# Performance work log

Hardware: AMD Instinct MI355X
Metric: run time of the kernel (lower is better)

The kernel has to match this reference:

```python
import jax, jax.numpy as jnp
import numpy as np

B, S, H, C = 2, 128, 768, 5
NEG = -1024.0

def setup_inputs() -> dict:
    key = jax.random.key(0)
    ks = jax.random.split(key, 6)
    sequence_output = jax.random.normal(ks[0], (B, S, H), dtype=jnp.float32)
    attention_mask = jnp.ones((B, S), dtype=jnp.int32)
    ng_token_mask = jax.random.bernoulli(ks[1], 0.5, (B, S, C, S))  # bool
    target = (jax.random.uniform(ks[2], (B, S, C, S)) < 0.01).astype(jnp.float32)
    lim = 1.0 / np.sqrt(H)
    W_prd = jax.random.uniform(ks[3], (H, H), jnp.float32, -lim, lim)
    b_prd = jnp.zeros((H,), jnp.float32)
    W_arg = jax.random.uniform(ks[4], (C * H, H), jnp.float32, -lim, lim)
    b_arg = jnp.zeros((C * H,), jnp.float32)
    W_out = jax.random.uniform(ks[5], (C, H), jnp.float32, -lim, lim)
    return dict(sequence_output=sequence_output, attention_mask=attention_mask,
                ng_token_mask=ng_token_mask, target=target,
                W_prd=W_prd, b_prd=b_prd, W_arg=W_arg, b_arg=b_arg, W_out=W_out)

def reference(sequence_output, attention_mask, ng_token_mask, target,
              W_prd, b_prd, W_arg, b_arg, W_out):
    b, s, h = sequence_output.shape
    c = W_out.shape[0]
    # get_mask: ng mask restricted to attended tokens, then any over case dim
    mask = ng_token_mask & (attention_mask[:, None, None, :] > 0)   # (B,S,C,S)
    mask = jnp.any(mask, axis=2, keepdims=True)                      # (B,S,1,S)
    # dropout is identity in eval mode
    h_p = sequence_output @ W_prd.T + b_prd                          # (B,S,H)
    h_a = (sequence_output @ W_arg.T + b_arg).reshape(b, s, c, h)    # (B,S,C,H)
    # outer-sum biaffine: (B, S_prd, S_arg, C, H)
    hh = jnp.tanh(h_p[:, :, None, None, :] + h_a[:, None, :, :, :])
    # per-case Linear(H,1,bias=False), stacked at dim=2 -> (B, S_prd, C, S_arg)
    output = jnp.einsum('bpach,ch->bpca', hh, W_out)
    output = output + (~mask).astype(output.dtype) * NEG
    # cross_entropy_pas_loss: multi-hot CE over candidate (last) axis
    log_sm = jax.nn.log_softmax(output, axis=3)
    loss = jnp.sum(-log_sm * target) / jnp.sum(target)
    return loss, output
```

## Files before the change

### kernel.cpp

```cpp
#include <hip/hip_runtime.h>
#include <math.h>

#define Bb 2
#define Ss 128
#define Hh 768
#define Cc 5
#define Mm 256
#define NEGV -1024.0f
#define SCALE 2.8853900817779268f

#define PT 2
#define NBLK (Mm / PT * Cc)

typedef __attribute__((ext_vector_type(8))) short bf16x8;
typedef __attribute__((ext_vector_type(4))) float f32x4;
typedef unsigned short ushort;

__device__ __forceinline__ unsigned pack_hi16(float hi, float lo) {
    return (__float_as_uint(hi) & 0xFFFF0000u) | (__float_as_uint(lo) >> 16);
}
__device__ __forceinline__ bf16x8 pack_bf16x8(float4 lo, float4 hi) {
    union { bf16x8 v; unsigned u[4]; } r;
    r.u[0] = pack_hi16(lo.y, lo.x);
    r.u[1] = pack_hi16(lo.w, lo.z);
    r.u[2] = pack_hi16(hi.y, hi.x);
    r.u[3] = pack_hi16(hi.w, hi.z);
    return r.v;
}

#define SB __builtin_amdgcn_sched_barrier(0);

__global__ __launch_bounds__(256)
void gemm_mfma(const float* __restrict__ X,
               const float* __restrict__ Wprd,
               const float* __restrict__ Warg,
               const float* __restrict__ bprd,
               const float* __restrict__ barg,
               float* __restrict__ EpG,
               ushort* __restrict__ haTb,
               float* __restrict__ accum)
{
    __shared__ __align__(16) ushort Asb[64][40];
    __shared__ __align__(16) ushort Bsb[32][40];

    if (blockIdx.x == 0 && blockIdx.y == 0 && threadIdx.x == 0) {
        accum[0] = 0.f; accum[1] = 0.f;
        ((unsigned*)accum)[2] = 0u;
    }
    const int bm   = blockIdx.x;
    const int bn   = blockIdx.y;
    const int tid  = threadIdx.x;
    const int wave = tid >> 6;
    const int lane = tid & 63;
    const int l16  = lane & 15;
    const int quad = lane >> 4;

    const float* Wsrc; const float* bsrc;
    const int nb = bn * 32;
    if (nb < Hh) { Wsrc = Wprd + (size_t)nb * Hh;        bsrc = bprd + nb; }
    else         { Wsrc = Warg + (size_t)(nb - Hh) * Hh; bsrc = barg + (nb - Hh); }

    const int srow = tid >> 2;
    const int sko  = (tid & 3) * 8;
    const float* gA = X + (size_t)(bm * 64 + srow) * Hh + sko;
    const float* gB = Wsrc + (size_t)(tid >> 2) * Hh + sko;

    float4 pa0 = *(const float4*)(gA);
    float4 pa1 = *(const float4*)(gA + 4);
    float4 pb0, pb1;
    if (tid < 128) { pb0 = *(const float4*)(gB); pb1 = *(const float4*)(gB + 4); }

    f32x4 acc0 = {0.f,0.f,0.f,0.f}, acc1 = {0.f,0.f,0.f,0.f};

    for (int k0 = 0; k0 < Hh; k0 += 32) {
        *(bf16x8*)&Asb[srow][sko] = pack_bf16x8(pa0, pa1);
        if (tid < 128) *(bf16x8*)&Bsb[tid >> 2][sko] = pack_bf16x8(pb0, pb1);
        __syncthreads();
        const int kn = k0 + 32;
        if (kn < Hh) {
            pa0 = *(const float4*)(gA + kn);
            pa1 = *(const float4*)(gA + kn + 4);
            if (tid < 128) { pb0 = *(const float4*)(gB + kn); pb1 = *(const float4*)(gB + kn + 4); }
        }
        bf16x8 af = *(const bf16x8*)&Asb[wave * 16 + l16][quad * 8];
        bf16x8 b0 = *(const bf16x8*)&Bsb[l16][quad * 8];
        bf16x8 b1 = *(const bf16x8*)&Bsb[16 + l16][quad * 8];
        acc0 = __builtin_amdgcn_mfma_f32_16x16x32_bf16(af, b0, acc0, 0, 0, 0);
        acc1 = __builtin_amdgcn_mfma_f32_16x16x32_bf16(af, b1, acc1, 0, 0, 0);
        __syncthreads();
    }

    const float sb0 = SCALE * bsrc[l16];
    const float sb1 = SCALE * bsrc[16 + l16];
    const int row = bm * 64 + wave * 16 + quad * 4;

    if (nb < Hh) {
        #pragma unroll
        for (int r = 0; r < 4; ++r) {
            const int mm = row + r;
            EpG[(size_t)mm * Hh + nb + l16]      = __builtin_amdgcn_exp2f(SCALE * acc0[r] + sb0);
            EpG[(size_t)mm * Hh + nb + 16 + l16] = __builtin_amdgcn_exp2f(SCALE * acc1[r] + sb1);
        }
    } else {
        const int q  = nb - Hh;
        const int cU = q / Hh;
        const int h0 = q % Hh;
        const int hA = h0 + l16;
        const int hB = h0 + 16 + l16;
        const size_t offA = (size_t)(hA >> 3) * 1024 + (hA & 7);
        const size_t offB = (size_t)(hB >> 3) * 1024 + (hB & 7);
        #pragma unroll
        for (int r = 0; r < 4; ++r) {
            const int mm = row + r;
            const int bI = mm >> 7, aI = mm & 127;
            const size_t base = ((size_t)(bI * Cc + cU) * 96) * 1024 + (size_t)aI * 8;
            const float v0 = SCALE * acc0[r] + sb0;
            const float v1 = SCALE * acc1[r] + sb1;
            haTb[base + offA] = (ushort)(__float_as_uint(v0) >> 16);
            haTb[base + offB] = (ushort)(__float_as_uint(v1) >> 16);
        }
    }
}

#define LOADG4(R, g) \
    R##0 = hap4[((g)*4+0)*128]; R##1 = hap4[((g)*4+1)*128]; \
    R##2 = hap4[((g)*4+2)*128]; R##3 = hap4[((g)*4+3)*128];

#define C1(u, hx) { \
    float w8[8], q0[8], q1[8]; \
    _Pragma("unroll") \
    for (int z = 0; z < 8; ++z) { \
        w8[z] = wrow[(hx) + z]; q0[z] = ep0[(hx) + z]; q1[z] = ep1[(hx) + z]; \
    } \
    const float e0 = __builtin_amdgcn_exp2f(__uint_as_float((u).x << 16)); \
    const float e1 = __builtin_amdgcn_exp2f(__uint_as_float((u).x & 0xFFFF0000u)); \
    const float e2 = __builtin_amdgcn_exp2f(__uint_as_float((u).y << 16)); \
    const float e3 = __builtin_amdgcn_exp2f(__uint_as_float((u).y & 0xFFFF0000u)); \
    const float e4 = __builtin_amdgcn_exp2f(__uint_as_float((u).z << 16)); \
    const float e5 = __builtin_amdgcn_exp2f(__uint_as_float((u).z & 0xFFFF0000u)); \
    const float e6 = __builtin_amdgcn_exp2f(__uint_as_float((u).w << 16)); \
    const float e7 = __builtin_amdgcn_exp2f(__uint_as_float((u).w & 0xFFFF0000u)); \
    float r; \
    r = __builtin_amdgcn_rcpf(fmaf(q0[0], e0, 1.0f)); ac00 = fmaf(w8[0], r, ac00); \
    r = __builtin_amdgcn_rcpf(fmaf(q0[1], e1, 1.0f)); ac01 = fmaf(w8[1], r, ac01); \
    r = __builtin_amdgcn_rcpf(fmaf(q0[2], e2, 1.0f)); ac00 = fmaf(w8[2], r, ac00); \
    r = __builtin_amdgcn_rcpf(fmaf(q0[3], e3, 1.0f)); ac01 = fmaf(w8[3], r, ac01); \
    r = __builtin_amdgcn_rcpf(fmaf(q0[4], e4, 1.0f)); ac00 = fmaf(w8[4], r, ac00); \
    r = __builtin_amdgcn_rcpf(fmaf(q0[5], e5, 1.0f)); ac01 = fmaf(w8[5], r, ac01); \
    r = __builtin_amdgcn_rcpf(fmaf(q0[6], e6, 1.0f)); ac00 = fmaf(w8[6], r, ac00); \
    r = __builtin_amdgcn_rcpf(fmaf(q0[7], e7, 1.0f)); ac01 = fmaf(w8[7], r, ac01); \
    r = __builtin_amdgcn_rcpf(fmaf(q1[0], e0, 1.0f)); ac10 = fmaf(w8[0], r, ac10); \
    r = __builtin_amdgcn_rcpf(fmaf(q1[1], e1, 1.0f)); ac11 = fmaf(w8[1], r, ac11); \
    r = __builtin_amdgcn_rcpf(fmaf(q1[2], e2, 1.0f)); ac10 = fmaf(w8[2], r, ac10); \
    r = __builtin_amdgcn_rcpf(fmaf(q1[3], e3, 1.0f)); ac11 = fmaf(w8[3], r, ac11); \
    r = __builtin_amdgcn_rcpf(fmaf(q1[4], e4, 1.0f)); ac10 = fmaf(w8[4], r, ac10); \
    r = __builtin_amdgcn_rcpf(fmaf(q1[5], e5, 1.0f)); ac11 = fmaf(w8[5], r, ac11); \
    r = __builtin_amdgcn_rcpf(fmaf(q1[6], e6, 1.0f)); ac10 = fmaf(w8[6], r, ac10); \
    r = __builtin_amdgcn_rcpf(fmaf(q1[7], e7, 1.0f)); ac11 = fmaf(w8[7], r, ac11); \
}

#define CONSUMEG4(R, g) \
    C1(R##0, hbase + ((g)*4+0)*8)  C1(R##1, hbase + ((g)*4+1)*8) \
    C1(R##2, hbase + ((g)*4+2)*8)  C1(R##3, hbase + ((g)*4+3)*8)

__global__ __launch_bounds__(512, 6)
void biaffine_loss(const float* __restrict__ EpG,
                   const ushort* __restrict__ haTb,
                   const float* __restrict__ Wout,
                   const int* __restrict__ ng,
                   const int* __restrict__ att,
                   const float* __restrict__ target,
                   float* __restrict__ out_logits,
                   float* __restrict__ accum,
                   float* __restrict__ out_loss)
{
    __shared__ float partial[PT][3][Ss];
    __shared__ float maskneg[PT][Ss];
    __shared__ float redmax[PT][2];
    __shared__ float red3[PT][2][3];
    __shared__ float swr_s;

    const int pt  = blockIdx.x / Cc;
    const int c   = blockIdx.x - pt * Cc;
    const int bp0 = pt * PT;
    const int b   = bp0 >> 7;
    const int tid = threadIdx.x;
    const int a   = tid & (Ss - 1);
    const int hq  = __builtin_amdgcn_readfirstlane(tid >> 7);
    const int lane = tid & 63;

    const float* wrow = Wout + (size_t)c * Hh;
    const float* ep0  = EpG + (size_t)(bp0 + 0) * Hh;
    const float* ep1  = EpG + (size_t)(bp0 + 1) * Hh;

    if (tid < PT * Ss) {
        const int p_i = tid >> 7;
        const int aa  = tid & (Ss - 1);
        int any = 0;
        if (att[b * Ss + aa] > 0) {
            const int* ngp = ng + (size_t)(bp0 + p_i) * Cc * Ss + aa;
            #pragma unroll
            for (int cc = 0; cc < Cc; ++cc) any |= ngp[cc * Ss];
        }
        maskneg[p_i][aa] = any ? 0.0f : NEGV;
    }

    if (tid < 64) {
        float s = 0.f;
        #pragma unroll
        for (int i = 0; i < Hh / 64; ++i) s += wrow[tid + i * 64];
        #pragma unroll
        for (int off = 32; off; off >>= 1) s += __shfl_xor(s, off, 64);
        if (tid == 0) swr_s = s;
    }

    const uint4* hap4 = (const uint4*)(haTb + ((size_t)(b * Cc + c) * 96) * 1024)
                      + (size_t)hq * 24 * 128 + a;
    const int hbase = hq * 192;

    uint4 A0, A1, A2, A3;
    uint4 B0, B1, B2, B3;
    float ac00 = 0.f, ac01 = 0.f, ac10 = 0.f, ac11 = 0.f;

    LOADG4(A, 0) SB
    LOADG4(B, 1) SB  CONSUMEG4(A, 0) SB
    LOADG4(A, 2) SB  CONSUMEG4(B, 1) SB
    LOADG4(B, 3) SB  CONSUMEG4(A, 2) SB
    LOADG4(A, 4) SB  CONSUMEG4(B, 3) SB
    LOADG4(B, 5) SB  CONSUMEG4(A, 4) SB
    CONSUMEG4(B, 5)

    if (hq != 0) {
        partial[0][hq - 1][a] = ac00 + ac01;
        partial[1][hq - 1][a] = ac10 + ac11;
    }
    __syncthreads();

    float logit[PT];
    const int wv = tid >> 6;
    if (hq == 0) {
        const float ps[PT] = { ac00 + ac01, ac10 + ac11 };
        #pragma unroll
        for (int p = 0; p < PT; ++p) {
            const float full = ps[p] + partial[p][0][a] + partial[p][1][a] + partial[p][2][a];
            logit[p] = swr_s - 2.0f * full + maskneg[p][a];
            out_logits[((size_t)(bp0 + p) * Cc + c) * Ss + a] = logit[p];
            float mx = logit[p];
            #pragma unroll
            for (int off = 32; off; off >>= 1) mx = fmaxf(mx, __shfl_xor(mx, off, 64));
            if (lane == 0) redmax[p][wv] = mx;
        }
    }
    __syncthreads();

    if (hq == 0) {
        #pragma unroll
        for (int p = 0; p < PT; ++p) {
            const float rm = fmaxf(redmax[p][0], redmax[p][1]);
            const float e  = __builtin_amdgcn_exp2f((logit[p] - rm) * 1.4426950408889634f);
            const float tg = target[((size_t)(bp0 + p) * Cc + c) * Ss + a];
            float se = e, st = tg, sx = tg * logit[p];
            #pragma unroll
            for (int off = 32; off; off >>= 1) {
                se += __shfl_xor(se, off, 64);
                st += __shfl_xor(st, off, 64);
                sx += __shfl_xor(sx, off, 64);
            }
            if (lane == 0) { red3[p][wv][0] = se; red3[p][wv][1] = st; red3[p][wv][2] = sx; }
        }
    }
    __syncthreads();

    if (tid == 0) {
        float nsum = 0.f, dsum = 0.f;
        #pragma unroll
        for (int p = 0; p < PT; ++p) {
            const float rm = fmaxf(redmax[p][0], redmax[p][1]);
            const float SE = red3[p][0][0] + red3[p][1][0];
            const float ST = red3[p][0][1] + red3[p][1][1];
            const float SX = red3[p][0][2] + red3[p][1][2];
            const float lse = rm + __builtin_amdgcn_logf(SE) * 0.6931471805599453f;
            nsum += lse * ST - SX;
            dsum += ST;
        }
        atomicAdd(&accum[0], nsum);
        atomicAdd(&accum[1], dsum);
        __threadfence();
        const unsigned old = atomicAdd((unsigned*)(accum + 2), 1u);
        if (old == (unsigned)(NBLK - 1)) {
            const float n = atomicAdd(&accum[0], 0.0f);
            const float d = atomicAdd(&accum[1], 0.0f);
            out_loss[0] = n / d;
        }
    }
}

extern "C" void kernel_launch(void* const* d_in, const int* in_sizes, int n_in,
                              void* d_out, int out_size, void* d_ws, size_t ws_size,
                              hipStream_t stream) {
    const float* seq    = (const float*)d_in[0];
    const int*   att    = (const int*)  d_in[1];
    const int*   ng     = (const int*)  d_in[2];
    const float* target = (const float*)d_in[3];
    const float* Wprd   = (const float*)d_in[4];
    const float* bprd   = (const float*)d_in[5];
    const float* Warg   = (const float*)d_in[6];
    const float* barg   = (const float*)d_in[7];
    const float* Wout   = (const float*)d_in[8];

    float*  out    = (float*)d_out;
    float*  EpG    = (float*)d_ws;
    ushort* haTb   = (ushort*)(EpG + 196608);
    float*  accum  = EpG + 196608 + 491520;

    gemm_mfma<<<dim3(4, 144), 256, 0, stream>>>(seq, Wprd, Warg, bprd, barg,
                                                EpG, haTb, accum);
    biaffine_loss<<<dim3(NBLK), 512, 0, stream>>>(EpG, haTb, Wout, ng, att, target,
                                                  out + 1, accum, out);
}
```

Before: 134.5 us.

## Precompute exp of arg projection in GEMM epilogue and double-buffer GEMM k-loop

The GEMM epilogue now stores exp2(scaled h_a) rounded to bf16 (round-to-nearest-even), so the biaffine inner loop no longer evaluates exp2 per element and only unpacks the bf16 values. This moves the exponential from the S×S×C×H inner loop to the much smaller S×C×H projection. The GEMM k-loop is also unrolled by two with separate prefetch register sets. Storing exp values in bf16 changes the rounding characteristics, and large exponents could overflow or lose precision.

```diff
diff --git a/kernel.cpp b/kernel.cpp
--- a/kernel.cpp
+++ b/kernel.cpp
@@ -27,8 +27,34 @@
     r.u[3] = pack_hi16(hi.w, hi.z);
     return r.v;
 }
+__device__ __forceinline__ ushort bf16_rne(float f) {
+    unsigned b = __float_as_uint(f);
+    return (ushort)((b + 0x7FFFu + ((b >> 16) & 1u)) >> 16);
+}
 
 #define SB __builtin_amdgcn_sched_barrier(0);
+
+
+#define GEMM_STEP(PA0, PA1, PB0, PB1, KNEXT) \
+    *(bf16x8*)&Asb[srow][sko] = pack_bf16x8(PA0, PA1); \
+    if (tid < 128) *(bf16x8*)&Bsb[tid >> 2][sko] = pack_bf16x8(PB0, PB1); \
+    __syncthreads(); \
+    if ((KNEXT) < Hh) { \
+        PA0 = *(const float4*)(gA + (KNEXT)); \
+        PA1 = *(const float4*)(gA + (KNEXT) + 4); \
+        if (tid < 128) { \
+            PB0 = *(const float4*)(gB + (KNEXT)); \
+            PB1 = *(const float4*)(gB + (KNEXT) + 4); \
+        } \
+    } \
+    { \
+        bf16x8 af = *(const bf16x8*)&Asb[wave * 16 + l16][quad * 8]; \
+        bf16x8 b0 = *(const bf16x8*)&Bsb[l16][quad * 8]; \
+        bf16x8 b1 = *(const bf16x8*)&Bsb[16 + l16][quad * 8]; \
+        acc0 = __builtin_amdgcn_mfma_f32_16x16x32_bf16(af, b0, acc0, 0, 0, 0); \
+        acc1 = __builtin_amdgcn_mfma_f32_16x16x32_bf16(af, b1, acc1, 0, 0, 0); \
+    } \
+    __syncthreads();
 
 __global__ __launch_bounds__(256)
 void gemm_mfma(const float* __restrict__ X,
@@ -65,29 +91,21 @@
     const float* gA = X + (size_t)(bm * 64 + srow) * Hh + sko;
     const float* gB = Wsrc + (size_t)(tid >> 2) * Hh + sko;
 
-    float4 pa0 = *(const float4*)(gA);
-    float4 pa1 = *(const float4*)(gA + 4);
-    float4 pb0, pb1;
-    if (tid < 128) { pb0 = *(const float4*)(gB); pb1 = *(const float4*)(gB + 4); }
+    float4 a00 = *(const float4*)(gA);
+    float4 a01 = *(const float4*)(gA + 4);
+    float4 a10 = *(const float4*)(gA + 32);
+    float4 a11 = *(const float4*)(gA + 36);
+    float4 b00, b01, b10, b11;
+    if (tid < 128) {
+        b00 = *(const float4*)(gB);      b01 = *(const float4*)(gB + 4);
+        b10 = *(const float4*)(gB + 32); b11 = *(const float4*)(gB + 36);
+    }
 
     f32x4 acc0 = {0.f,0.f,0.f,0.f}, acc1 = {0.f,0.f,0.f,0.f};
 
-    for (int k0 = 0; k0 < Hh; k0 += 32) {
-        *(bf16x8*)&Asb[srow][sko] = pack_bf16x8(pa0, pa1);
-        if (tid < 128) *(bf16x8*)&Bsb[tid >> 2][sko] = pack_bf16x8(pb0, pb1);
-        __syncthreads();
-        const int kn = k0 + 32;
-        if (kn < Hh) {
-            pa0 = *(const float4*)(gA + kn);
-            pa1 = *(const float4*)(gA + kn + 4);
-            if (tid < 128) { pb0 = *(const float4*)(gB + kn); pb1 = *(const float4*)(gB + kn + 4); }
-        }
-        bf16x8 af = *(const bf16x8*)&Asb[wave * 16 + l16][quad * 8];
-        bf16x8 b0 = *(const bf16x8*)&Bsb[l16][quad * 8];
-        bf16x8 b1 = *(const bf16x8*)&Bsb[16 + l16][quad * 8];
-        acc0 = __builtin_amdgcn_mfma_f32_16x16x32_bf16(af, b0, acc0, 0, 0, 0);
-        acc1 = __builtin_amdgcn_mfma_f32_16x16x32_bf16(af, b1, acc1, 0, 0, 0);
-        __syncthreads();
+    for (int k0 = 0; k0 < Hh; k0 += 64) {
+        GEMM_STEP(a00, a01, b00, b01, k0 + 64)
+        GEMM_STEP(a10, a11, b10, b11, k0 + 96)
     }
 
     const float sb0 = SCALE * bsrc[l16];
@@ -114,10 +132,10 @@
             const int mm = row + r;
             const int bI = mm >> 7, aI = mm & 127;
             const size_t base = ((size_t)(bI * Cc + cU) * 96) * 1024 + (size_t)aI * 8;
-            const float v0 = SCALE * acc0[r] + sb0;
-            const float v1 = SCALE * acc1[r] + sb1;
-            haTb[base + offA] = (ushort)(__float_as_uint(v0) >> 16);
-            haTb[base + offB] = (ushort)(__float_as_uint(v1) >> 16);
+            const float e0 = __builtin_amdgcn_exp2f(SCALE * acc0[r] + sb0);
+            const float e1 = __builtin_amdgcn_exp2f(SCALE * acc1[r] + sb1);
+            haTb[base + offA] = bf16_rne(e0);
+            haTb[base + offB] = bf16_rne(e1);
         }
     }
 }
@@ -132,14 +150,14 @@
     for (int z = 0; z < 8; ++z) { \
         w8[z] = wrow[(hx) + z]; q0[z] = ep0[(hx) + z]; q1[z] = ep1[(hx) + z]; \
     } \
-    const float e0 = __builtin_amdgcn_exp2f(__uint_as_float((u).x << 16)); \
-    const float e1 = __builtin_amdgcn_exp2f(__uint_as_float((u).x & 0xFFFF0000u)); \
-    const float e2 = __builtin_amdgcn_exp2f(__uint_as_float((u).y << 16)); \
-    const float e3 = __builtin_amdgcn_exp2f(__uint_as_float((u).y & 0xFFFF0000u)); \
-    const float e4 = __builtin_amdgcn_exp2f(__uint_as_float((u).z << 16)); \
-    const float e5 = __builtin_amdgcn_exp2f(__uint_as_float((u).z & 0xFFFF0000u)); \
-    const float e6 = __builtin_amdgcn_exp2f(__uint_as_float((u).w << 16)); \
-    const float e7 = __builtin_amdgcn_exp2f(__uint_as_float((u).w & 0xFFFF0000u)); \
+    const float e0 = __uint_as_float((u).x << 16); \
+    const float e1 = __uint_as_float((u).x & 0xFFFF0000u); \
+    const float e2 = __uint_as_float((u).y << 16); \
+    const float e3 = __uint_as_float((u).y & 0xFFFF0000u); \
+    const float e4 = __uint_as_float((u).z << 16); \
+    const float e5 = __uint_as_float((u).z & 0xFFFF0000u); \
+    const float e6 = __uint_as_float((u).w << 16); \
+    const float e7 = __uint_as_float((u).w & 0xFFFF0000u); \
     float r; \
     r = __builtin_amdgcn_rcpf(fmaf(q0[0], e0, 1.0f)); ac00 = fmaf(w8[0], r, ac00); \
     r = __builtin_amdgcn_rcpf(fmaf(q0[1], e1, 1.0f)); ac01 = fmaf(w8[1], r, ac01); \
```

Result: faster. 128.9 us (-4.1%).
